# Optimization experiments

Hardware: AMD Instinct MI355X
Metric: run time of the kernel (lower is better)

## Reference

```python
import jax, jax.numpy as jnp
import numpy as np

B, H, W, R, C = 4, 64, 64, 64, 32  # batch, height, width, in-channels r, conv out-channels


def setup_inputs() -> dict:
    key = jax.random.key(0)
    kx, kf, kg = jax.random.split(key, 3)
    x = jax.random.normal(kx, (B, H, W, R), dtype=jnp.float32)
    # 1x1 conv with in_channels=1: kernel is effectively a length-C vector
    w_f = jax.random.normal(kf, (C,), dtype=jnp.float32) * 0.1
    w_g = jax.random.normal(kg, (C,), dtype=jnp.float32) * 0.1
    gamma = jnp.ones((), dtype=jnp.float32)
    return {"x": x, "w_f": w_f, "w_g": w_g, "gamma": gamma}


def reference(x, w_f, w_g, gamma):
    b, h, w, r = x.shape
    hw = h * w
    xs = x.reshape(b, hw, r)                      # [B, HW, R]
    # conv_f / conv_g: each scalar of xs times weight vector -> [B, HW, R*C]
    x_f = (xs[..., None] * w_f).reshape(b, hw, -1)
    x_g = (xs[..., None] * w_g).reshape(b, hw, -1)
    attn = jnp.einsum('bik,bjk->bij', x_f, x_g)   # [B, HW, HW]
    attn = jax.nn.softmax(attn, axis=-1) * gamma
    # out[b,j,r] = sum_i attn[b,j,i] * xs[b,i,r]
    out = jnp.einsum('bji,bir->bjr', attn, xs)
    return out.reshape(b, h, w, r)
```

## Files before the change

### kernel.cpp

```cpp
#include <hip/hip_runtime.h>


#define N_SEQ 4096
#define KS    3
#define LOG2E 1.4426950408889634f
#define LDP2  72

typedef __attribute__((ext_vector_type(8))) short short8;
typedef __attribute__((ext_vector_type(4))) short short4v;
typedef __attribute__((ext_vector_type(4))) float f4;
typedef _Float16 half8  __attribute__((ext_vector_type(8)));
typedef _Float16 half4v __attribute__((ext_vector_type(4)));
typedef _Float16 half2t __attribute__((ext_vector_type(2)));
typedef __fp16   fp16x2 __attribute__((ext_vector_type(2)));

union U8  { short8 v8; short4v v4[2]; unsigned short u[8]; };
union HU8 { half8 v; half2t h2[4]; unsigned short u[8]; };
union HU4 { half4v v; half2t h2[2]; unsigned short u[4]; };
union PK  { fp16x2 f; half2t h; };

#define MFMA16(a,b,c) __builtin_amdgcn_mfma_f32_16x16x32_bf16(a,b,c,0,0,0)
#define MFMAH(a,b,c)  __builtin_amdgcn_mfma_f32_16x16x32_f16(a,b,c,0,0,0)

static __device__ __forceinline__ unsigned short f2bf(float f){
  unsigned int u = __float_as_uint(f);
  u += 0x7fffu + ((u>>16)&1u);
  return (unsigned short)(u>>16);
}
static __device__ __forceinline__ float bf2f(unsigned short b){
  return __uint_as_float(((unsigned int)b)<<16);
}
static __device__ __forceinline__ half2t pkrtz(float a, float b){
#if __has_builtin(__builtin_amdgcn_cvt_pkrtz)
  PK u; u.f = __builtin_amdgcn_cvt_pkrtz(a, b);
  return u.h;
#else
  half2t r; r.x = (_Float16)a; r.y = (_Float16)b; return r;
#endif
}
static __device__ __forceinline__ float fexp2(float x){
#if __has_builtin(__builtin_amdgcn_exp2f)
  return __builtin_amdgcn_exp2f(x);
#else
  return exp2f(x);
#endif
}
static __device__ __forceinline__ f4 splat4(float v){ f4 r; r.x=v; r.y=v; r.z=v; r.w=v; return r; }
static __device__ __forceinline__ f4 exp2v(f4 v){
  f4 r; r.x=fexp2(v.x); r.y=fexp2(v.y); r.z=fexp2(v.z); r.w=fexp2(v.w); return r;
}
static __device__ __forceinline__ f4 max4(f4 a, f4 b){
  f4 r; r.x=fmaxf(a.x,b.x); r.y=fmaxf(a.y,b.y); r.z=fmaxf(a.z,b.z); r.w=fmaxf(a.w,b.w); return r;
}
static __device__ __forceinline__ f4 shx4(f4 v, int m){
  f4 r; r.x=__shfl_xor(v.x,m,64); r.y=__shfl_xor(v.y,m,64);
        r.z=__shfl_xor(v.z,m,64); r.w=__shfl_xor(v.w,m,64); return r;
}

__global__ __launch_bounds__(256) void prep_kernel(
    const float* __restrict__ x, unsigned short* __restrict__ xh,
    unsigned short* __restrict__ xt)
{
  __shared__ unsigned short T[64][66];
  const int tid = threadIdx.x;
  const int bb  = blockIdx.x >> 6;
  const int n0  = (blockIdx.x & 63) << 6;
  {
    const int r  = tid >> 2;
    const int c4 = tid & 3;
    const float* src = x + ((size_t)(bb*N_SEQ + n0 + r))*64 + c4*16;
    unsigned short h[16];
    #pragma unroll
    for (int i = 0; i < 4; ++i) {
      const float4 f = *(const float4*)(src + i*4);
      HU4 u; u.h2[0] = pkrtz(f.x, f.y); u.h2[1] = pkrtz(f.z, f.w);
      h[i*4+0]=u.u[0]; h[i*4+1]=u.u[1]; h[i*4+2]=u.u[2]; h[i*4+3]=u.u[3];
    }
    unsigned short* dst = xh + ((size_t)(bb*N_SEQ + n0 + r))*64 + c4*16;
    U8 u0, u1;
    #pragma unroll
    for (int j = 0; j < 8; ++j) { u0.u[j]=h[j]; u1.u[j]=h[8+j]; }
    *(short8*)dst = u0.v8; *(short8*)(dst+8) = u1.v8;
    #pragma unroll
    for (int j = 0; j < 16; ++j) T[r][c4*16+j] = h[j];
  }
  __syncthreads();
  {
    const int d = tid >> 2;
    const int g = tid & 3;
    unsigned short o[16];
    #pragma unroll
    for (int j = 0; j < 16; ++j) o[j] = T[g*16+j][d];
    unsigned short* dst = xt + ((size_t)(bb*64 + d))*N_SEQ + n0 + g*16;
    U8 u0, u1;
    #pragma unroll
    for (int j = 0; j < 8; ++j) { u0.u[j]=o[j]; u1.u[j]=o[8+j]; }
    *(short8*)dst = u0.v8; *(short8*)(dst+8) = u1.v8;
  }
}

__global__ __launch_bounds__(256, 3) void fattn3_kernel(
    const float* __restrict__ x, const float* __restrict__ wf,
    const float* __restrict__ wg,
    const unsigned short* __restrict__ xh, const unsigned short* __restrict__ xt,
    float* __restrict__ OP, float* __restrict__ LP)
{
  __shared__ __align__(16) unsigned short KH[2][4096];
  __shared__ __align__(16) unsigned short VT[2][4096];
  __shared__ __align__(16) unsigned short PB[4][32*LDP2];

  const int tid  = threadIdx.x;
  const int lane = tid & 63;
  const int wv   = tid >> 6;
  const int mg   = wv & 1;
  const int hh   = wv >> 1;
  const int quad = lane >> 4;
  const int l15  = lane & 15;
  const int swz  = l15 & 7;
  const int ks   = blockIdx.x >> 8;
  const int rem  = blockIdx.x & 255;
  const int bb   = rem >> 6;
  const int qb   = (rem & 63) << 6;

  const int t0 = (ks == 0) ? 0 : (22 + 21*(ks-1));
  const int t1 = t0 + ((ks == 0) ? 22 : 21);
  const int NIT = 11;

  float s = 0.f;
  #pragma unroll
  for (int i = 0; i < 32; ++i) s += wf[i]*wg[i];
  const float s2 = s * LOG2E;

  const float* xb = x + ((size_t)bb * N_SEQ) * 64;

  half8 qf[2][2];
  #pragma unroll
  for (int mt = 0; mt < 2; ++mt) {
    const int row = qb + mg*32 + mt*16 + l15;
    #pragma unroll
    for (int c = 0; c < 2; ++c) {
      const float* src = xb + row*64 + c*32 + quad*8;
      const float4 a0 = *(const float4*)src;
      const float4 a1 = *(const float4*)(src+4);
      HU8 u;
      u.h2[0] = pkrtz(a0.x*s2, a0.y*s2);
      u.h2[1] = pkrtz(a0.z*s2, a0.w*s2);
      u.h2[2] = pkrtz(a1.x*s2, a1.y*s2);
      u.h2[3] = pkrtz(a1.z*s2, a1.w*s2);
      qf[mt][c] = u.v;
    }
  }

  f4 Oc[2][4];
  f4 lsa[2];
  #pragma unroll
  for (int mt = 0; mt < 2; ++mt) {
    lsa[mt] = splat4(0.f);
    #pragma unroll
    for (int nt = 0; nt < 4; ++nt) Oc[mt][nt] = splat4(0.f);
  }

  unsigned short* PBw = PB[wv];

  int srr[8], scg[8];
  #pragma unroll
  for (int i = 0; i < 8; ++i) {
    const int ch = wv*2 + (i & 1);
    const int p  = ch*64 + lane;
    srr[i] = p >> 3;
    scg[i] = (p & 7) ^ (srr[i] & 7);
  }

  short8 sr[8];

  #pragma unroll
  for (int i = 0; i < 8; ++i) {
    const int h   = (i >> 1) & 1;
    const int tIx = min(t0 + h, t1 - 1);
    const int kg  = tIx * 64;
    if ((i >> 1) < 2)
      sr[i] = *(const short8*)(xh + ((size_t)(bb*N_SEQ + kg + srr[i]))*64 + scg[i]*8);
    else
      sr[i] = *(const short8*)(xt + ((size_t)(bb*64 + srr[i]))*N_SEQ + kg + scg[i]*8);
  }

  #pragma unroll 1
  for (int it = 0; it < NIT; ++it) {
    #pragma unroll
    for (int i = 0; i < 8; ++i) {
      const int ch = wv*2 + (i & 1);
      const int p  = ch*64 + lane;
      unsigned short* base = ((i >> 1) < 2) ? &KH[(i>>1)&1][0] : &VT[(i>>1)&1][0];
      *(short8*)(base + p*8) = sr[i];
    }
    __syncthreads();

    if (it + 1 < NIT) {
      #pragma unroll
      for (int i = 0; i < 8; ++i) {
        const int h   = (i >> 1) & 1;
        const int tIx = min(t0 + (it+1)*2 + h, t1 - 1);
        const int kg  = tIx * 64;
        if ((i >> 1) < 2)
          sr[i] = *(const short8*)(xh + ((size_t)(bb*N_SEQ + kg + srr[i]))*64 + scg[i]*8);
        else
          sr[i] = *(const short8*)(xt + ((size_t)(bb*64 + srr[i]))*N_SEQ + kg + scg[i]*8);
      }
    }

    const bool valid = (t0 + it*2 + hh) < t1;
    if (valid) {
      f4 St[4][2];
      #pragma unroll
      for (int k2 = 0; k2 < 4; ++k2)
        #pragma unroll
        for (int mt = 0; mt < 2; ++mt) St[k2][mt] = splat4(0.f);

      #pragma unroll
      for (int c = 0; c < 2; ++c) {
        half8 kf[4];
        #pragma unroll
        for (int k2 = 0; k2 < 4; ++k2)
          kf[k2] = *(const half8*)&KH[hh][(k2*16 + l15)*64 + (((c*4 + quad) ^ swz))*8];
        #pragma unroll
        for (int k2 = 0; k2 < 4; ++k2)
          #pragma unroll
          for (int mt = 0; mt < 2; ++mt)
            St[k2][mt] = MFMAH(kf[k2], qf[mt][c], St[k2][mt]);
      }

      #pragma unroll
      for (int k2 = 0; k2 < 4; ++k2) {
        #pragma unroll
        for (int mt = 0; mt < 2; ++mt) {
          const f4 p = exp2v(St[k2][mt]);
          lsa[mt] += p;
          HU4 u; u.h2[0] = pkrtz(p.x, p.y); u.h2[1] = pkrtz(p.z, p.w);
          *(half4v*)&PBw[(mt*16 + l15)*LDP2 + k2*16 + quad*4] = u.v;
        }
      }

      #pragma unroll
      for (int kc = 0; kc < 2; ++kc) {
        half8 pa[2];
        #pragma unroll
        for (int mt = 0; mt < 2; ++mt)
          pa[mt] = *(const half8*)&PBw[(mt*16 + l15)*LDP2 + kc*32 + quad*8];
        #pragma unroll
        for (int nt = 0; nt < 4; ++nt) {
          const half8 vb = *(const half8*)&VT[hh][(nt*16 + l15)*64 + (((kc*4 + quad) ^ swz))*8];
          #pragma unroll
          for (int mt = 0; mt < 2; ++mt)
            Oc[mt][nt] = MFMAH(pa[mt], vb, Oc[mt][nt]);
        }
      }
    }
    __syncthreads();
  }

  float lsum[2];
  #pragma unroll
  for (int mt = 0; mt < 2; ++mt) {
    float sv = lsa[mt].x + lsa[mt].y + lsa[mt].z + lsa[mt].w;
    sv += __shfl_xor(sv, 16, 64);
    sv += __shfl_xor(sv, 32, 64);
    lsum[mt] = sv;
  }

  float* MO = (float*)KH;
  float* ML = (float*)VT;
  if (hh == 1) {
    #pragma unroll
    for (int mt = 0; mt < 2; ++mt) {
      const int rbase = mg*32 + mt*16 + quad*4;
      #pragma unroll
      for (int nt = 0; nt < 4; ++nt) {
        MO[(rbase+0)*64 + nt*16 + l15] = Oc[mt][nt].x;
        MO[(rbase+1)*64 + nt*16 + l15] = Oc[mt][nt].y;
        MO[(rbase+2)*64 + nt*16 + l15] = Oc[mt][nt].z;
        MO[(rbase+3)*64 + nt*16 + l15] = Oc[mt][nt].w;
      }
      if (quad == 0) ML[mg*32 + mt*16 + l15] = lsum[mt];
    }
  }
  __syncthreads();
  if (hh == 0) {
    float* op = OP + (size_t)blockIdx.x * 4096;
    #pragma unroll
    for (int mt = 0; mt < 2; ++mt) {
      const int rbase = mg*32 + mt*16 + quad*4;
      #pragma unroll
      for (int nt = 0; nt < 4; ++nt) {
        #pragma unroll
        for (int rg = 0; rg < 4; ++rg) {
          const int rr = rbase + rg;
          op[rr*64 + nt*16 + l15] = Oc[mt][nt][rg] + MO[rr*64 + nt*16 + l15];
        }
      }
      if (quad == 0)
        LP[(size_t)blockIdx.x*64 + mg*32 + mt*16 + l15] = lsum[mt] + ML[mg*32 + mt*16 + l15];
    }
  }
}

__global__ __launch_bounds__(256) void merge_kernel(
    const float* __restrict__ OP, const float* __restrict__ LP,
    const float* __restrict__ gm, float* __restrict__ out)
{
  const int idx = blockIdx.x*256 + threadIdx.x;
  const int e0  = idx*4;
  const int d0  = e0 & 63;
  const int row = e0 >> 6;
  const int bb  = row >> 12;
  const int q   = row & 4095;
  const int qt  = q >> 6;
  const int qr  = q & 63;
  float4 acc = make_float4(0.f,0.f,0.f,0.f);
  float l = 0.f;
  #pragma unroll
  for (int sct = 0; sct < KS; ++sct) {
    const int blk = sct*256 + bb*64 + qt;
    const float4 o = *(const float4*)(OP + (size_t)blk*4096 + qr*64 + d0);
    acc.x += o.x; acc.y += o.y; acc.z += o.z; acc.w += o.w;
    l += LP[(size_t)blk*64 + qr];
  }
  const float w = gm[0] / l;
  float4 r; r.x = acc.x*w; r.y = acc.y*w; r.z = acc.z*w; r.w = acc.w*w;
  *(float4*)(out + e0) = r;
}

#define LDKF 72
#define TILEF (64*LDKF)
#define LDP 36

__global__ __launch_bounds__(256) void fattn_fallback(
    const float* __restrict__ x, const float* __restrict__ wf,
    const float* __restrict__ wg, const float* __restrict__ gm,
    float* __restrict__ out)
{
  __shared__ __align__(16) unsigned short KHI[2*TILEF];
  __shared__ __align__(16) unsigned short KLO[2*TILEF];
  __shared__ __align__(16) unsigned short VT [2*TILEF];
  __shared__ __align__(16) unsigned short PB [4*32*LDP];

  const int tid  = threadIdx.x;
  const int lane = tid & 63;
  const int wv   = tid >> 6;
  const int mg   = wv & 1;
  const int hh   = wv >> 1;
  const int quad = lane >> 4;
  const int l15  = lane & 15;
  const int bb   = blockIdx.x >> 6;
  const int qb   = (blockIdx.x & 63) << 6;

  float s = 0.f;
  #pragma unroll
  for (int i = 0; i < 32; ++i) s += wf[i]*wg[i];
  const float s2 = s * LOG2E;
  const float gamma = gm[0];

  const float* xb = x + ((size_t)bb * N_SEQ) * 64;

  short8 qhf[2][2], qlf[2][2];
  #pragma unroll
  for (int mt = 0; mt < 2; ++mt) {
    const int row = qb + mg*32 + mt*16 + l15;
    #pragma unroll
    for (int c = 0; c < 2; ++c) {
      const float* src = xb + row*64 + c*32 + quad*8;
      const float4 a0 = *(const float4*)src;
      const float4 a1 = *(const float4*)(src+4);
      float qv[8] = {a0.x,a0.y,a0.z,a0.w,a1.x,a1.y,a1.z,a1.w};
      U8 vh, vl;
      #pragma unroll
      for (int j = 0; j < 8; ++j) {
        float q = qv[j]*s2;
        unsigned short hb = f2bf(q);
        vh.u[j] = (short)hb;
        vl.u[j] = (short)f2bf(q - bf2f(hb));
      }
      qhf[mt][c] = vh.v8; qlf[mt][c] = vl.v8;
    }
  }

  f4 Oc[2][4], mo[2], ls[2];
  #pragma unroll
  for (int mt = 0; mt < 2; ++mt) {
    mo[mt] = splat4(-1e30f);
    ls[mt] = splat4(0.f);
    #pragma unroll
    for (int nt = 0; nt < 4; ++nt) Oc[mt][nt] = splat4(0.f);
  }

  const int sh   = tid >> 7;
  const int srow = (tid & 127) >> 1;
  const int sch  = tid & 1;

  float4 sr[8];
  {
    const float* sp = xb + (sh*2048 + srow)*64 + sch*32;
    #pragma unroll
    for (int i = 0; i < 8; ++i) sr[i] = *(const float4*)(sp + i*4);
    unsigned short hb[32], lb[32];
    #pragma unroll
    for (int i = 0; i < 8; ++i) {
      float vv[4] = {sr[i].x, sr[i].y, sr[i].z, sr[i].w};
      #pragma unroll
      for (int j = 0; j < 4; ++j) {
        unsigned short h = f2bf(vv[j]);
        hb[i*4+j] = h;
        lb[i*4+j] = f2bf(vv[j] - bf2f(h));
      }
    }
    const int kbase = sh*TILEF + srow*LDKF + sch*32;
    #pragma unroll
    for (int g = 0; g < 4; ++g) {
      U8 wh, wl;
      #pragma unroll
      for (int j = 0; j < 8; ++j) { wh.u[j]=(short)hb[g*8+j]; wl.u[j]=(short)lb[g*8+j]; }
      *(short8*)&KHI[kbase+g*8] = wh.v8;
      *(short8*)&KLO[kbase+g*8] = wl.v8;
    }
    #pragma unroll
    for (int j = 0; j < 32; ++j) VT[sh*TILEF + (sch*32+j)*LDKF + srow] = hb[j];
  }
  __syncthreads();

  #pragma unroll 1
  for (int t = 0; t < 32; ++t) {
    if (t+1 < 32) {
      const float* sp = xb + (sh*2048 + (t+1)*64 + srow)*64 + sch*32;
      #pragma unroll
      for (int i = 0; i < 8; ++i) sr[i] = *(const float4*)(sp + i*4);
    }

    f4 Sa[2][4];
    #pragma unroll
    for (int mt = 0; mt < 2; ++mt)
      #pragma unroll
      for (int n = 0; n < 4; ++n) Sa[mt][n] = splat4(0.f);

    const int kldsb = hh*TILEF;
    #pragma unroll
    for (int n = 0; n < 4; ++n) {
      #pragma unroll
      for (int c = 0; c < 2; ++c) {
        const int off = kldsb + (n*16 + l15)*LDKF + c*32 + quad*8;
        const short8 bh = *(const short8*)&KHI[off];
        const short8 bl = *(const short8*)&KLO[off];
        #pragma unroll
        for (int mt = 0; mt < 2; ++mt) {
          Sa[mt][n] = MFMA16(qhf[mt][c], bh, Sa[mt][n]);
          Sa[mt][n] = MFMA16(qlf[mt][c], bh, Sa[mt][n]);
          Sa[mt][n] = MFMA16(qhf[mt][c], bl, Sa[mt][n]);
        }
      }
    }

    f4 p[2][4];
    #pragma unroll
    for (int mt = 0; mt < 2; ++mt) {
      f4 rm = max4(max4(Sa[mt][0],Sa[mt][1]), max4(Sa[mt][2],Sa[mt][3]));
      rm = max4(rm, shx4(rm,1));
      rm = max4(rm, shx4(rm,2));
      rm = max4(rm, shx4(rm,4));
      rm = max4(rm, shx4(rm,8));
      f4 mn = max4(mo[mt], rm);
      f4 al = exp2v(mo[mt] - mn);
      mo[mt] = mn;
      f4 rs = splat4(0.f);
      #pragma unroll
      for (int n = 0; n < 4; ++n) { p[mt][n] = exp2v(Sa[mt][n] - mn); rs += p[mt][n]; }
      rs += shx4(rs,1); rs += shx4(rs,2); rs += shx4(rs,4); rs += shx4(rs,8);
      ls[mt] = ls[mt]*al + rs;
      #pragma unroll
      for (int nt = 0; nt < 4; ++nt) Oc[mt][nt] *= al;
    }

    const int pw = wv * (32*LDP);
    #pragma unroll
    for (int kc = 0; kc < 2; ++kc) {
      #pragma unroll
      for (int mt = 0; mt < 2; ++mt) {
        #pragma unroll
        for (int n2 = 0; n2 < 2; ++n2) {
          const f4 pv = p[mt][kc*2+n2];
          const int base = pw + (mt*16 + quad*4)*LDP + n2*16 + l15;
          ((unsigned short*)PB)[base        ] = f2bf(pv.x);
          ((unsigned short*)PB)[base +   LDP] = f2bf(pv.y);
          ((unsigned short*)PB)[base + 2*LDP] = f2bf(pv.z);
          ((unsigned short*)PB)[base + 3*LDP] = f2bf(pv.w);
        }
      }
      short8 pa[2];
      #pragma unroll
      for (int mt = 0; mt < 2; ++mt) {
        U8 u;
        const int rb = pw + (mt*16 + l15)*LDP + quad*8;
        u.v4[0] = *(const short4v*)&((unsigned short*)PB)[rb];
        u.v4[1] = *(const short4v*)&((unsigned short*)PB)[rb+4];
        pa[mt] = u.v8;
      }
      #pragma unroll
      for (int nt = 0; nt < 4; ++nt) {
        const short8 vb = *(const short8*)&VT[kldsb + (nt*16 + l15)*LDKF + kc*32 + quad*8];
        #pragma unroll
        for (int mt = 0; mt < 2; ++mt) Oc[mt][nt] = MFMA16(pa[mt], vb, Oc[mt][nt]);
      }
    }

    __syncthreads();

    if (t+1 < 32) {
      unsigned short hb[32], lb[32];
      #pragma unroll
      for (int i = 0; i < 8; ++i) {
        float vv[4] = {sr[i].x, sr[i].y, sr[i].z, sr[i].w};
        #pragma unroll
        for (int j = 0; j < 4; ++j) {
          unsigned short h = f2bf(vv[j]);
          hb[i*4+j] = h;
          lb[i*4+j] = f2bf(vv[j] - bf2f(h));
        }
      }
      const int kbase = sh*TILEF + srow*LDKF + sch*32;
      #pragma unroll
      for (int g = 0; g < 4; ++g) {
        U8 wh, wl;
        #pragma unroll
        for (int j = 0; j < 8; ++j) { wh.u[j]=(short)hb[g*8+j]; wl.u[j]=(short)lb[g*8+j]; }
        *(short8*)&KHI[kbase+g*8] = wh.v8;
        *(short8*)&KLO[kbase+g*8] = wl.v8;
      }
      #pragma unroll
      for (int j = 0; j < 32; ++j) VT[sh*TILEF + (sch*32+j)*LDKF + srow] = hb[j];
      __syncthreads();
    }
  }

  float* MO  = (float*)KHI;
  float* MML = (float*)KLO;
  if (hh == 1) {
    #pragma unroll
    for (int mt = 0; mt < 2; ++mt) {
      const int rbase = mg*32 + mt*16 + quad*4;
      #pragma unroll
      for (int nt = 0; nt < 4; ++nt) {
        MO[(rbase+0)*64 + nt*16 + l15] = Oc[mt][nt].x;
        MO[(rbase+1)*64 + nt*16 + l15] = Oc[mt][nt].y;
        MO[(rbase+2)*64 + nt*16 + l15] = Oc[mt][nt].z;
        MO[(rbase+3)*64 + nt*16 + l15] = Oc[mt][nt].w;
      }
      if (l15 == 0) {
        MML[rbase+0] = mo[mt].x; MML[rbase+1] = mo[mt].y;
        MML[rbase+2] = mo[mt].z; MML[rbase+3] = mo[mt].w;
        MML[64+rbase+0] = ls[mt].x; MML[64+rbase+1] = ls[mt].y;
        MML[64+rbase+2] = ls[mt].z; MML[64+rbase+3] = ls[mt].w;
      }
    }
  }
  __syncthreads();
  if (hh == 0) {
    #pragma unroll
    for (int mt = 0; mt < 2; ++mt) {
      const int rbase = mg*32 + mt*16 + quad*4;
      f4 m1, l1;
      m1.x = MML[rbase+0]; m1.y = MML[rbase+1]; m1.z = MML[rbase+2]; m1.w = MML[rbase+3];
      l1.x = MML[64+rbase+0]; l1.y = MML[64+rbase+1]; l1.z = MML[64+rbase+2]; l1.w = MML[64+rbase+3];
      const f4 mn = max4(mo[mt], m1);
      const f4 a0 = exp2v(mo[mt] - mn);
      const f4 a1 = exp2v(m1 - mn);
      f4 lt = ls[mt]*a0 + l1*a1;
      f4 w; w.x = gamma/lt.x; w.y = gamma/lt.y; w.z = gamma/lt.z; w.w = gamma/lt.w;
      #pragma unroll
      for (int nt = 0; nt < 4; ++nt) {
        #pragma unroll
        for (int rg = 0; rg < 4; ++rg) {
          const int rr = rbase + rg;
          const float o1 = MO[rr*64 + nt*16 + l15];
          const float val = (Oc[mt][nt][rg]*a0[rg] + o1*a1[rg]) * w[rg];
          out[((size_t)bb*N_SEQ + qb + rr)*64 + nt*16 + l15] = val;
        }
      }
    }
  }
}

extern "C" void kernel_launch(void* const* d_in, const int* in_sizes, int n_in,
                              void* d_out, int out_size, void* d_ws, size_t ws_size,
                              hipStream_t stream) {
  const float* x  = (const float*)d_in[0];
  const float* wf = (const float*)d_in[1];
  const float* wg = (const float*)d_in[2];
  const float* gm = (const float*)d_in[3];
  float* out = (float*)d_out;

  const size_t XH_OFF = 0;
  const size_t XT_OFF = 2097152;
  const size_t OP_OFF = 4194304;
  const size_t LP_OFF = OP_OFF + (size_t)KS*256*4096*4;
  const size_t NEED   = LP_OFF + (size_t)KS*256*64*4;

  if (ws_size >= NEED) {
    unsigned short* xhp = (unsigned short*)((char*)d_ws + XH_OFF);
    unsigned short* xtp = (unsigned short*)((char*)d_ws + XT_OFF);
    float* OP = (float*)((char*)d_ws + OP_OFF);
    float* LP = (float*)((char*)d_ws + LP_OFF);
    prep_kernel<<<dim3(256), dim3(256), 0, stream>>>(x, xhp, xtp);
    fattn3_kernel<<<dim3(KS*256), dim3(256), 0, stream>>>(x, wf, wg, xhp, xtp, OP, LP);
    merge_kernel<<<dim3(1024), dim3(256), 0, stream>>>(OP, LP, gm, out);
  } else {
    fattn_fallback<<<dim3(256), dim3(256), 0, stream>>>(x, wf, wg, gm, out);
  }
}
```

Before: 95.95 us.

## Restructure attention around 32x32 MFMA with register-resident P and async LDS loads

Prep now writes x as fp16 pre-tiled into MFMA fragment order for both K and transposed V, so the attention kernel can issue contiguous per-lane loads. The attention kernel moves to 512-thread blocks with 64 queries per wave, 32x32x16 f16 MFMAs, and a KV split of 8 instead of 3. Direct global-to-LDS loads are double-buffered, and the softmax probabilities are rearranged into A-operand fragments with lane shuffles instead of going through an LDS staging buffer. The goal is to raise MFMA density and cut LDS round trips, at the cost of larger partial-output buffers and a heavier merge pass. Softmax still skips max subtraction, as it did before.

```diff
diff --git a/kernel.cpp b/kernel.cpp
--- a/kernel.cpp
+++ b/kernel.cpp
@@ -2,25 +2,24 @@
 
 
 #define N_SEQ 4096
-#define KS    3
+#define KS    8
 #define LOG2E 1.4426950408889634f
-#define LDP2  72
 
 typedef __attribute__((ext_vector_type(8))) short short8;
 typedef __attribute__((ext_vector_type(4))) short short4v;
 typedef __attribute__((ext_vector_type(4))) float f4;
+typedef __attribute__((ext_vector_type(16))) float f32x16;
 typedef _Float16 half8  __attribute__((ext_vector_type(8)));
-typedef _Float16 half4v __attribute__((ext_vector_type(4)));
 typedef _Float16 half2t __attribute__((ext_vector_type(2)));
 typedef __fp16   fp16x2 __attribute__((ext_vector_type(2)));
 
 union U8  { short8 v8; short4v v4[2]; unsigned short u[8]; };
-union HU8 { half8 v; half2t h2[4]; unsigned short u[8]; };
-union HU4 { half4v v; half2t h2[2]; unsigned short u[4]; };
-union PK  { fp16x2 f; half2t h; };
-
-#define MFMA16(a,b,c) __builtin_amdgcn_mfma_f32_16x16x32_bf16(a,b,c,0,0,0)
-#define MFMAH(a,b,c)  __builtin_amdgcn_mfma_f32_16x16x32_f16(a,b,c,0,0,0)
+union PKU { fp16x2 f; half2t h; unsigned int u; };
+union US  { short8 s; half8 h; };
+union W4U { unsigned int u[4]; half8 h; };
+
+#define MFMA16(a,b,c)  __builtin_amdgcn_mfma_f32_16x16x32_bf16(a,b,c,0,0,0)
+#define MFMA32F(a,b,c) __builtin_amdgcn_mfma_f32_32x32x16_f16(a,b,c,0,0,0)
 
 static __device__ __forceinline__ unsigned short f2bf(float f){
   unsigned int u = __float_as_uint(f);
@@ -30,12 +29,11 @@
 static __device__ __forceinline__ float bf2f(unsigned short b){
   return __uint_as_float(((unsigned int)b)<<16);
 }
-static __device__ __forceinline__ half2t pkrtz(float a, float b){
+static __device__ __forceinline__ unsigned int pk_u32(float a, float b){
 #if __has_builtin(__builtin_amdgcn_cvt_pkrtz)
-  PK u; u.f = __builtin_amdgcn_cvt_pkrtz(a, b);
-  return u.h;
+  PKU u; u.f = __builtin_amdgcn_cvt_pkrtz(a, b); return u.u;
 #else
-  half2t r; r.x = (_Float16)a; r.y = (_Float16)b; return r;
+  PKU u; u.h.x = (_Float16)a; u.h.y = (_Float16)b; return u.u;
 #endif
 }
 static __device__ __forceinline__ float fexp2(float x){
@@ -56,273 +54,233 @@
   f4 r; r.x=__shfl_xor(v.x,m,64); r.y=__shfl_xor(v.y,m,64);
         r.z=__shfl_xor(v.z,m,64); r.w=__shfl_xor(v.w,m,64); return r;
 }
-
-__global__ __launch_bounds__(256) void prep_kernel(
-    const float* __restrict__ x, unsigned short* __restrict__ xh,
-    unsigned short* __restrict__ xt)
+static __device__ __forceinline__ f32x16 zero16(){
+  f32x16 z;
+  #pragma unroll
+  for (int i = 0; i < 16; ++i) z[i] = 0.f;
+  return z;
+}
+static __device__ __forceinline__ void gload16(const unsigned short* g, unsigned short* l){
+  __builtin_amdgcn_global_load_lds((const __attribute__((address_space(1))) void*)g,
+                                   (__attribute__((address_space(3))) void*)l, 16, 0, 0);
+}
+static __device__ __forceinline__ half8 mkfrag(unsigned int Da0, unsigned int Da1,
+                                               unsigned int Db0, unsigned int Db1, bool hib){
+  const unsigned int e0 = __shfl_xor(hib ? Da0 : Db0, 32, 64);
+  const unsigned int e1 = __shfl_xor(hib ? Da1 : Db1, 32, 64);
+  W4U w;
+  w.u[0] = hib ? e0  : Da0;
+  w.u[1] = hib ? e1  : Da1;
+  w.u[2] = hib ? Db0 : e0;
+  w.u[3] = hib ? Db1 : e1;
+  return w.h;
+}
+
+__global__ __launch_bounds__(256) void prep6_kernel(
+    const float* __restrict__ x,
+    unsigned short* __restrict__ XF, unsigned short* __restrict__ VF)
 {
-  __shared__ unsigned short T[64][66];
-  const int tid = threadIdx.x;
-  const int bb  = blockIdx.x >> 6;
-  const int n0  = (blockIdx.x & 63) << 6;
+  __shared__ __align__(16) unsigned short T [64][80];
+  __shared__ __align__(16) unsigned short TT[64][80];
+  const int tid  = threadIdx.x;
+  const int bb   = blockIdx.x >> 6;
+  const int tile = blockIdx.x & 63;
   {
     const int r  = tid >> 2;
     const int c4 = tid & 3;
-    const float* src = x + ((size_t)(bb*N_SEQ + n0 + r))*64 + c4*16;
+    const float* src = x + ((size_t)(bb*N_SEQ + tile*64 + r))*64 + c4*16;
     unsigned short h[16];
     #pragma unroll
     for (int i = 0; i < 4; ++i) {
       const float4 f = *(const float4*)(src + i*4);
-      HU4 u; u.h2[0] = pkrtz(f.x, f.y); u.h2[1] = pkrtz(f.z, f.w);
-      h[i*4+0]=u.u[0]; h[i*4+1]=u.u[1]; h[i*4+2]=u.u[2]; h[i*4+3]=u.u[3];
-    }
-    unsigned short* dst = xh + ((size_t)(bb*N_SEQ + n0 + r))*64 + c4*16;
-    U8 u0, u1;
-    #pragma unroll
-    for (int j = 0; j < 8; ++j) { u0.u[j]=h[j]; u1.u[j]=h[8+j]; }
-    *(short8*)dst = u0.v8; *(short8*)(dst+8) = u1.v8;
+      const unsigned int u0 = pk_u32(f.x, f.y);
+      const unsigned int u1 = pk_u32(f.z, f.w);
+      h[i*4+0] = (unsigned short)(u0 & 0xffffu);
+      h[i*4+1] = (unsigned short)(u0 >> 16);
+      h[i*4+2] = (unsigned short)(u1 & 0xffffu);
+      h[i*4+3] = (unsigned short)(u1 >> 16);
+    }
     #pragma unroll
     for (int j = 0; j < 16; ++j) T[r][c4*16+j] = h[j];
+    #pragma unroll
+    for (int j = 0; j < 16; ++j) TT[c4*16+j][r] = h[j];
   }
   __syncthreads();
-  {
-    const int d = tid >> 2;
-    const int g = tid & 3;
-    unsigned short o[16];
-    #pragma unroll
-    for (int j = 0; j < 16; ++j) o[j] = T[g*16+j][d];
-    unsigned short* dst = xt + ((size_t)(bb*64 + d))*N_SEQ + n0 + g*16;
-    U8 u0, u1;
-    #pragma unroll
-    for (int j = 0; j < 8; ++j) { u0.u[j]=o[j]; u1.u[j]=o[8+j]; }
-    *(short8*)dst = u0.v8; *(short8*)(dst+8) = u1.v8;
-  }
-}
-
-__global__ __launch_bounds__(256, 3) void fattn3_kernel(
-    const float* __restrict__ x, const float* __restrict__ wf,
-    const float* __restrict__ wg,
-    const unsigned short* __restrict__ xh, const unsigned short* __restrict__ xt,
+  const size_t ob = ((size_t)(bb*64 + tile)) * 4096;
+  #pragma unroll
+  for (int s0 = 0; s0 < 2; ++s0) {
+    const int s  = s0*256 + tid;
+    const int fb = s >> 6;
+    const int l  = s & 63;
+    const int rr = (fb >> 2)*32 + (l & 31);
+    const int cc = (fb & 3)*16 + (l >> 5)*8;
+    *(short8*)(XF + ob + (size_t)s*8) = *(const short8*)&T [rr][cc];
+    *(short8*)(VF + ob + (size_t)s*8) = *(const short8*)&TT[rr][cc];
+  }
+}
+
+__global__ __launch_bounds__(512, 2) void fattn6_kernel(
+    const float* __restrict__ wf, const float* __restrict__ wg,
+    const unsigned short* __restrict__ XF, const unsigned short* __restrict__ VF,
     float* __restrict__ OP, float* __restrict__ LP)
 {
-  __shared__ __align__(16) unsigned short KH[2][4096];
-  __shared__ __align__(16) unsigned short VT[2][4096];
-  __shared__ __align__(16) unsigned short PB[4][32*LDP2];
+  __shared__ __align__(16) unsigned short KL[2][4096];
+  __shared__ __align__(16) unsigned short VL[2][4096];
 
   const int tid  = threadIdx.x;
   const int lane = tid & 63;
   const int wv   = tid >> 6;
-  const int mg   = wv & 1;
-  const int hh   = wv >> 1;
-  const int quad = lane >> 4;
-  const int l15  = lane & 15;
-  const int swz  = l15 & 7;
-  const int ks   = blockIdx.x >> 8;
-  const int rem  = blockIdx.x & 255;
-  const int bb   = rem >> 6;
-  const int qb   = (rem & 63) << 6;
-
-  const int t0 = (ks == 0) ? 0 : (22 + 21*(ks-1));
-  const int t1 = t0 + ((ks == 0) ? 22 : 21);
-  const int NIT = 11;
+  const int l31  = lane & 31;
+  const int hi   = lane >> 5;
+  const bool hib = hi != 0;
+  const int ks   = blockIdx.x >> 5;
+  const int rem  = blockIdx.x & 31;
+  const int bb   = rem >> 3;
+  const int qB   = rem & 7;
 
   float s = 0.f;
   #pragma unroll
   for (int i = 0; i < 32; ++i) s += wf[i]*wg[i];
   const float s2 = s * LOG2E;
-
-  const float* xb = x + ((size_t)bb * N_SEQ) * 64;
-
-  half8 qf[2][2];
-  #pragma unroll
-  for (int mt = 0; mt < 2; ++mt) {
-    const int row = qb + mg*32 + mt*16 + l15;
-    #pragma unroll
-    for (int c = 0; c < 2; ++c) {
-      const float* src = xb + row*64 + c*32 + quad*8;
-      const float4 a0 = *(const float4*)src;
-      const float4 a1 = *(const float4*)(src+4);
-      HU8 u;
-      u.h2[0] = pkrtz(a0.x*s2, a0.y*s2);
-      u.h2[1] = pkrtz(a0.z*s2, a0.w*s2);
-      u.h2[2] = pkrtz(a1.x*s2, a1.y*s2);
-      u.h2[3] = pkrtz(a1.z*s2, a1.w*s2);
-      qf[mt][c] = u.v;
-    }
-  }
-
-  f4 Oc[2][4];
-  f4 lsa[2];
-  #pragma unroll
-  for (int mt = 0; mt < 2; ++mt) {
-    lsa[mt] = splat4(0.f);
-    #pragma unroll
-    for (int nt = 0; nt < 4; ++nt) Oc[mt][nt] = splat4(0.f);
-  }
-
-  unsigned short* PBw = PB[wv];
-
-  int srr[8], scg[8];
-  #pragma unroll
-  for (int i = 0; i < 8; ++i) {
-    const int ch = wv*2 + (i & 1);
-    const int p  = ch*64 + lane;
-    srr[i] = p >> 3;
-    scg[i] = (p & 7) ^ (srr[i] & 7);
-  }
-
-  short8 sr[8];
-
-  #pragma unroll
-  for (int i = 0; i < 8; ++i) {
-    const int h   = (i >> 1) & 1;
-    const int tIx = min(t0 + h, t1 - 1);
-    const int kg  = tIx * 64;
-    if ((i >> 1) < 2)
-      sr[i] = *(const short8*)(xh + ((size_t)(bb*N_SEQ + kg + srr[i]))*64 + scg[i]*8);
-    else
-      sr[i] = *(const short8*)(xt + ((size_t)(bb*64 + srr[i]))*N_SEQ + kg + scg[i]*8);
-  }
+  const _Float16 s2h = (_Float16)s2;
+
+  half8 qf[2][4];
+  {
+    const unsigned short* xq = XF + ((size_t)(bb*64 + qB*8 + wv))*4096 + lane*8;
+    half8 sv;
+    #pragma unroll
+    for (int j = 0; j < 8; ++j) sv[j] = s2h;
+    #pragma unroll
+    for (int qg = 0; qg < 2; ++qg)
+      #pragma unroll
+      for (int kst = 0; kst < 4; ++kst) {
+        US u; u.s = *(const short8*)(xq + (qg*4+kst)*512);
+        qf[qg][kst] = u.h * sv;
+      }
+  }
+
+  f32x16 Oc[2][2];
+  #pragma unroll
+  for (int qg = 0; qg < 2; ++qg)
+    #pragma unroll
+    for (int dg = 0; dg < 2; ++dg) Oc[qg][dg] = zero16();
+  float lacc[2] = {0.f, 0.f};
+
+  const unsigned short* gK = XF + ((size_t)(bb*64 + ks*8))*4096 + wv*512 + lane*8;
+  const unsigned short* gV = VF + ((size_t)(bb*64 + ks*8))*4096 + wv*512 + lane*8;
+  unsigned short* lK0 = &KL[0][wv*512];
+  unsigned short* lV0 = &VL[0][wv*512];
+  unsigned short* lK1 = &KL[1][wv*512];
+  unsigned short* lV1 = &VL[1][wv*512];
+
+  gload16(gK, lK0);
+  gload16(gV, lV0);
+  __syncthreads();
 
   #pragma unroll 1
-  for (int it = 0; it < NIT; ++it) {
-    #pragma unroll
-    for (int i = 0; i < 8; ++i) {
-      const int ch = wv*2 + (i & 1);
-      const int p  = ch*64 + lane;
-      unsigned short* base = ((i >> 1) < 2) ? &KH[(i>>1)&1][0] : &VT[(i>>1)&1][0];
-      *(short8*)(base + p*8) = sr[i];
+  for (int it = 0; it < 8; ++it) {
+    const int cur = it & 1;
+    if (it + 1 < 8) {
+      gload16(gK + (it+1)*4096, cur ? lK0 : lK1);
+      gload16(gV + (it+1)*4096, cur ? lV0 : lV1);
+    }
+    const unsigned short* KB = &KL[cur][0];
+    const unsigned short* VB = &VL[cur][0];
+
+    #pragma unroll
+    for (int kg = 0; kg < 2; ++kg) {
+      half8 kf[4];
+      #pragma unroll
+      for (int kst = 0; kst < 4; ++kst) {
+        US u; u.s = *(const short8*)(KB + ((kg*4+kst)*64 + lane)*8);
+        kf[kst] = u.h;
+      }
+      f32x16 St[2];
+      St[0] = zero16(); St[1] = zero16();
+      __builtin_amdgcn_s_setprio(1);
+      #pragma unroll
+      for (int kst = 0; kst < 4; ++kst) {
+        St[0] = MFMA32F(kf[kst], qf[0][kst], St[0]);
+        St[1] = MFMA32F(kf[kst], qf[1][kst], St[1]);
+      }
+      __builtin_amdgcn_s_setprio(0);
+
+      half8 pa[2][2];
+      #pragma unroll
+      for (int qg = 0; qg < 2; ++qg) {
+        float p[16];
+        float sm = 0.f;
+        #pragma unroll
+        for (int r = 0; r < 16; ++r) { p[r] = fexp2(St[qg][r]); sm += p[r]; }
+        lacc[qg] += sm;
+        const unsigned int D0 = pk_u32(p[0],  p[1]);
+        const unsigned int D1 = pk_u32(p[2],  p[3]);
+        const unsigned int D2 = pk_u32(p[4],  p[5]);
+        const unsigned int D3 = pk_u32(p[6],  p[7]);
+        const unsigned int D4 = pk_u32(p[8],  p[9]);
+        const unsigned int D5 = pk_u32(p[10], p[11]);
+        const unsigned int D6 = pk_u32(p[12], p[13]);
+        const unsigned int D7 = pk_u32(p[14], p[15]);
+        pa[qg][0] = mkfrag(D0, D1, D2, D3, hib);
+        pa[qg][1] = mkfrag(D4, D5, D6, D7, hib);
+      }
+
+      __builtin_amdgcn_s_setprio(1);
+      #pragma unroll
+      for (int dg = 0; dg < 2; ++dg) {
+        US v0, v1;
+        v0.s = *(const short8*)(VB + ((dg*4 + kg*2 + 0)*64 + lane)*8);
+        v1.s = *(const short8*)(VB + ((dg*4 + kg*2 + 1)*64 + lane)*8);
+        #pragma unroll
+        for (int qg = 0; qg < 2; ++qg) {
+          Oc[qg][dg] = MFMA32F(pa[qg][0], v0.h, Oc[qg][dg]);
+          Oc[qg][dg] = MFMA32F(pa[qg][1], v1.h, Oc[qg][dg]);
+        }
+      }
+      __builtin_amdgcn_s_setprio(0);
     }
     __syncthreads();
-
-    if (it + 1 < NIT) {
-      #pragma unroll
-      for (int i = 0; i < 8; ++i) {
-        const int h   = (i >> 1) & 1;
-        const int tIx = min(t0 + (it+1)*2 + h, t1 - 1);
-        const int kg  = tIx * 64;
-        if ((i >> 1) < 2)
-          sr[i] = *(const short8*)(xh + ((size_t)(bb*N_SEQ + kg + srr[i]))*64 + scg[i]*8);
-        else
-          sr[i] = *(const short8*)(xt + ((size_t)(bb*64 + srr[i]))*N_SEQ + kg + scg[i]*8);
-      }
-    }
-
-    const bool valid = (t0 + it*2 + hh) < t1;
-    if (valid) {
-      f4 St[4][2];
-      #pragma unroll
-      for (int k2 = 0; k2 < 4; ++k2)
-        #pragma unroll
-        for (int mt = 0; mt < 2; ++mt) St[k2][mt] = splat4(0.f);
-
-      #pragma unroll
-      for (int c = 0; c < 2; ++c) {
-        half8 kf[4];
-        #pragma unroll
-        for (int k2 = 0; k2 < 4; ++k2)
-          kf[k2] = *(const half8*)&KH[hh][(k2*16 + l15)*64 + (((c*4 + quad) ^ swz))*8];
-        #pragma unroll
-        for (int k2 = 0; k2 < 4; ++k2)
-          #pragma unroll
-          for (int mt = 0; mt < 2; ++mt)
-            St[k2][mt] = MFMAH(kf[k2], qf[mt][c], St[k2][mt]);
-      }
-
-      #pragma unroll
-      for (int k2 = 0; k2 < 4; ++k2) {
-        #pragma unroll
-        for (int mt = 0; mt < 2; ++mt) {
-          const f4 p = exp2v(St[k2][mt]);
-          lsa[mt] += p;
-          HU4 u; u.h2[0] = pkrtz(p.x, p.y); u.h2[1] = pkrtz(p.z, p.w);
-          *(half4v*)&PBw[(mt*16 + l15)*LDP2 + k2*16 + quad*4] = u.v;
-        }
-      }
-
-      #pragma unroll
-      for (int kc = 0; kc < 2; ++kc) {
-        half8 pa[2];
-        #pragma unroll
-        for (int mt = 0; mt < 2; ++mt)
-          pa[mt] = *(const half8*)&PBw[(mt*16 + l15)*LDP2 + kc*32 + quad*8];
-        #pragma unroll
-        for (int nt = 0; nt < 4; ++nt) {
-          const half8 vb = *(const half8*)&VT[hh][(nt*16 + l15)*64 + (((kc*4 + quad) ^ swz))*8];
-          #pragma unroll
-          for (int mt = 0; mt < 2; ++mt)
-            Oc[mt][nt] = MFMAH(pa[mt], vb, Oc[mt][nt]);
-        }
-      }
-    }
-    __syncthreads();
-  }
-
-  float lsum[2];
-  #pragma unroll
-  for (int mt = 0; mt < 2; ++mt) {
-    float sv = lsa[mt].x + lsa[mt].y + lsa[mt].z + lsa[mt].w;
-    sv += __shfl_xor(sv, 16, 64);
-    sv += __shfl_xor(sv, 32, 64);
-    lsum[mt] = sv;
-  }
-
-  float* MO = (float*)KH;
-  float* ML = (float*)VT;
-  if (hh == 1) {
-    #pragma unroll
-    for (int mt = 0; mt < 2; ++mt) {
-      const int rbase = mg*32 + mt*16 + quad*4;
-      #pragma unroll
-      for (int nt = 0; nt < 4; ++nt) {
-        MO[(rbase+0)*64 + nt*16 + l15] = Oc[mt][nt].x;
-        MO[(rbase+1)*64 + nt*16 + l15] = Oc[mt][nt].y;
-        MO[(rbase+2)*64 + nt*16 + l15] = Oc[mt][nt].z;
-        MO[(rbase+3)*64 + nt*16 + l15] = Oc[mt][nt].w;
-      }
-      if (quad == 0) ML[mg*32 + mt*16 + l15] = lsum[mt];
-    }
-  }
-  __syncthreads();
-  if (hh == 0) {
-    float* op = OP + (size_t)blockIdx.x * 4096;
-    #pragma unroll
-    for (int mt = 0; mt < 2; ++mt) {
-      const int rbase = mg*32 + mt*16 + quad*4;
-      #pragma unroll
-      for (int nt = 0; nt < 4; ++nt) {
-        #pragma unroll
-        for (int rg = 0; rg < 4; ++rg) {
-          const int rr = rbase + rg;
-          op[rr*64 + nt*16 + l15] = Oc[mt][nt][rg] + MO[rr*64 + nt*16 + l15];
-        }
-      }
-      if (quad == 0)
-        LP[(size_t)blockIdx.x*64 + mg*32 + mt*16 + l15] = lsum[mt] + ML[mg*32 + mt*16 + l15];
-    }
-  }
-}
-
-__global__ __launch_bounds__(256) void merge_kernel(
+  }
+
+  lacc[0] += __shfl_xor(lacc[0], 32, 64);
+  lacc[1] += __shfl_xor(lacc[1], 32, 64);
+
+  float* op = OP + (size_t)blockIdx.x * (512*64);
+  #pragma unroll
+  for (int qg = 0; qg < 2; ++qg) {
+    #pragma unroll
+    for (int dg = 0; dg < 2; ++dg) {
+      #pragma unroll
+      for (int r = 0; r < 16; ++r) {
+        const int row = wv*64 + qg*32 + (r & 3) + 8*(r >> 2) + 4*hi;
+        op[row*64 + dg*32 + l31] = Oc[qg][dg][r];
+      }
+    }
+    if (hi == 0)
+      LP[(size_t)blockIdx.x*512 + wv*64 + qg*32 + l31] = lacc[qg];
+  }
+}
+
+__global__ __launch_bounds__(256) void merge6_kernel(
     const float* __restrict__ OP, const float* __restrict__ LP,
     const float* __restrict__ gm, float* __restrict__ out)
 {
   const int idx = blockIdx.x*256 + threadIdx.x;
   const int e0  = idx*4;
   const int d0  = e0 & 63;
-  const int row = e0 >> 6;
-  const int bb  = row >> 12;
-  const int q   = row & 4095;
-  const int qt  = q >> 6;
-  const int qr  = q & 63;
+  const int q   = e0 >> 6;
+  const int bb  = q >> 12;
+  const int qq  = q & 4095;
+  const int qB  = qq >> 9;
+  const int row = qq & 511;
   float4 acc = make_float4(0.f,0.f,0.f,0.f);
   float l = 0.f;
   #pragma unroll
   for (int sct = 0; sct < KS; ++sct) {
-    const int blk = sct*256 + bb*64 + qt;
-    const float4 o = *(const float4*)(OP + (size_t)blk*4096 + qr*64 + d0);
+    const int blk = sct*32 + bb*8 + qB;
+    const float4 o = *(const float4*)(OP + (size_t)blk*32768 + row*64 + d0);
     acc.x += o.x; acc.y += o.y; acc.z += o.z; acc.w += o.w;
-    l += LP[(size_t)blk*64 + qr];
+    l += LP[(size_t)blk*512 + row];
   }
   const float w = gm[0] / l;
   float4 r; r.x = acc.x*w; r.y = acc.y*w; r.z = acc.z*w; r.w = acc.w*w;
@@ -595,20 +553,20 @@
   const float* gm = (const float*)d_in[3];
   float* out = (float*)d_out;
 
-  const size_t XH_OFF = 0;
-  const size_t XT_OFF = 2097152;
+  const size_t XF_OFF = 0;
+  const size_t VF_OFF = 2097152;
   const size_t OP_OFF = 4194304;
-  const size_t LP_OFF = OP_OFF + (size_t)KS*256*4096*4;
-  const size_t NEED   = LP_OFF + (size_t)KS*256*64*4;
+  const size_t LP_OFF = OP_OFF + (size_t)256*512*64*4;
+  const size_t NEED   = LP_OFF + (size_t)256*512*4;
 
   if (ws_size >= NEED) {
-    unsigned short* xhp = (unsigned short*)((char*)d_ws + XH_OFF);
-    unsigned short* xtp = (unsigned short*)((char*)d_ws + XT_OFF);
+    unsigned short* XFp = (unsigned short*)((char*)d_ws + XF_OFF);
+    unsigned short* VFp = (unsigned short*)((char*)d_ws + VF_OFF);
     float* OP = (float*)((char*)d_ws + OP_OFF);
     float* LP = (float*)((char*)d_ws + LP_OFF);
-    prep_kernel<<<dim3(256), dim3(256), 0, stream>>>(x, xhp, xtp);
-    fattn3_kernel<<<dim3(KS*256), dim3(256), 0, stream>>>(x, wf, wg, xhp, xtp, OP, LP);
-    merge_kernel<<<dim3(1024), dim3(256), 0, stream>>>(OP, LP, gm, out);
+    prep6_kernel<<<dim3(256), dim3(256), 0, stream>>>(x, XFp, VFp);
+    fattn6_kernel<<<dim3(256), dim3(512), 0, stream>>>(wf, wg, XFp, VFp, OP, LP);
+    merge6_kernel<<<dim3(1024), dim3(256), 0, stream>>>(OP, LP, gm, out);
   } else {
     fattn_fallback<<<dim3(256), dim3(256), 0, stream>>>(x, wf, wg, gm, out);
   }
```

Measured after the change: 91.91 us (median of 2 runs). 4.2% less time.
